# Optimization experiments

Measured on AMD Instinct MI355X. Metric: run time of the kernel, lower is better.

## Reference

```python
import jax, jax.numpy as jnp
import numpy as np

MODES = 12

def _conv3x3_circular(x, w, b):
    # x: [B,C,H,W], w: [O,I,3,3] -> circular padding of 1 then VALID conv
    xp = jnp.pad(x, ((0, 0), (0, 0), (1, 1), (1, 1)), mode='wrap')
    y = jax.lax.conv_general_dilated(xp, w, window_strides=(1, 1), padding='VALID',
                                     dimension_numbers=('NCHW', 'OIHW', 'NCHW'))
    return y + b[None, :, None, None]

def _spectral_conv(x, w1, w2):
    # x: [B,C,H,W] real; w1, w2: [C,O,m1,m2] complex
    B, C, H, W = x.shape
    x_ft = jnp.fft.rfft2(x)  # [B,C,H,W//2+1] complex
    m1 = min(MODES, H // 2)
    m2 = min(MODES, W // 2 + 1)
    top = jnp.einsum('bixy,ioxy->boxy', x_ft[:, :, :m1, :m2], w1[:, :, :m1, :m2])
    bot = jnp.einsum('bixy,ioxy->boxy', x_ft[:, :, -m1:, :m2], w2[:, :, :m1, :m2])
    out_ft = jnp.zeros((B, w1.shape[1], H, W // 2 + 1), dtype=x_ft.dtype)
    out_ft = out_ft.at[:, :, :m1, :m2].set(top).at[:, :, -m1:, :m2].set(bot)
    return jnp.fft.irfft2(out_ft, s=(H, W))

def setup_inputs() -> dict:
    key = jax.random.key(0)
    ks = jax.random.split(key, 16)
    width = 32
    scale = 1.0 / (width * width)
    return {
        'x': jax.random.normal(ks[0], (64, 2, 128, 128), dtype=jnp.float32),
        'p_w': jax.random.normal(ks[1], (width, 2, 3, 3), dtype=jnp.float32) * 0.2,
        'p_b': jax.random.normal(ks[2], (width,), dtype=jnp.float32) * 0.1,
        'scw1r': jax.random.uniform(ks[3], (4, width, width, MODES, MODES), dtype=jnp.float32) * scale,
        'scw1i': jax.random.uniform(ks[4], (4, width, width, MODES, MODES), dtype=jnp.float32) * scale,
        'scw2r': jax.random.uniform(ks[5], (4, width, width, MODES, MODES), dtype=jnp.float32) * scale,
        'scw2i': jax.random.uniform(ks[6], (4, width, width, MODES, MODES), dtype=jnp.float32) * scale,
        'ww': jax.random.normal(ks[7], (4, width, width), dtype=jnp.float32) * (1.0 / np.sqrt(width)),
        'wb': jax.random.normal(ks[8], (4, width), dtype=jnp.float32) * 0.1,
        'q1_w': jax.random.normal(ks[9], (128, width), dtype=jnp.float32) * (1.0 / np.sqrt(width)),
        'q1_b': jax.random.normal(ks[10], (128,), dtype=jnp.float32) * 0.1,
        'q2_w': jax.random.normal(ks[11], (1, 128), dtype=jnp.float32) * (1.0 / np.sqrt(128.0)),
        'q2_b': jax.random.normal(ks[12], (1,), dtype=jnp.float32) * 0.1,
    }

def reference(x, p_w, p_b, scw1r, scw1i, scw2r, scw2i, ww, wb, q1_w, q1_b, q2_w, q2_b):
    h = _conv3x3_circular(x, p_w, p_b)  # lifting: [B,2,H,W] -> [B,width,H,W]
    for i in range(4):
        w1 = scw1r[i] + 1j * scw1i[i]
        w2 = scw2r[i] + 1j * scw2i[i]
        x1 = _spectral_conv(h, w1, w2)
        x2 = jnp.einsum('bihw,oi->bohw', h, ww[i]) + wb[i][None, :, None, None]
        h = jax.nn.gelu(x1 + x2, approximate=False)
    g = h.mean(axis=(2, 3))  # [B,width]
    g = jax.nn.gelu(g @ q1_w.T + q1_b, approximate=False)
    g = g @ q2_w.T + q2_b
    return jax.nn.sigmoid(g)
```

## Files before the change

### kernel.cpp

```cpp
#include <hip/hip_runtime.h>
#include <math.h>

#define B 64
#define CIN 2
#define CH 32
#define H 128
#define W 128
#define MODES 12
#define KY 24
#define KX 12
#define HW (H*W)
#define NMODE (KY*KX)

typedef float f32x2 __attribute__((ext_vector_type(2)));
__device__ __forceinline__ f32x2 mk2(float a, float b) { f32x2 r; r.x = a; r.y = b; return r; }

__device__ __forceinline__ float gelu_f(float x) {
    float ax = fabsf(x) * 0.70710678118654752f;
    float t  = __builtin_amdgcn_rcpf(1.0f + 0.3275911f * ax);
    float p  = t * (0.254829592f + t * (-0.284496736f + t * (1.421413741f +
               t * (-1.453152027f + t * 1.061405429f))));
    float e  = __expf(-ax * ax);
    float er = copysignf(1.0f - p * e, x);
    return 0.5f * x * (1.0f + er);
}

__global__ __launch_bounds__(256) void k_init_tables(
        float* cWkw, float* sWkw, float* cnsWkw,
        float* cnsH2, float* mnsH2) {
    int t = blockIdx.x * 256 + threadIdx.x;
    const float TWO_PI_OVER = 6.283185307179586476925f / 128.0f;
    if (t < MODES * W) {
        int k = t / W, w = t % W;
        int m = (k * w) & 127;
        float s, c;
        sincosf(TWO_PI_OVER * (float)m, &s, &c);
        cWkw[k * W + w] = c;  sWkw[k * W + w] = s;
        cnsWkw[(k * W + w) * 2]     = c;
        cnsWkw[(k * W + w) * 2 + 1] = -s;
    } else if (t < MODES * W + KY * H) {
        int u = t - MODES * W;
        int kyI = u / H, hh = u % H;
        int ky = (kyI < MODES) ? kyI : (H - MODES + (kyI - MODES));
        int m = (ky * hh) & 127;
        float s, c;
        sincosf(TWO_PI_OVER * (float)m, &s, &c);
        cnsH2[(hh * KY + kyI) * 2]     = c;
        cnsH2[(hh * KY + kyI) * 2 + 1] = s;
        mnsH2[(hh * KY + kyI) * 2]     = -s;
        mnsH2[(hh * KY + kyI) * 2 + 1] = c;
    }
}

__global__ __launch_bounds__(256) void k_reorder_w(
        const float* __restrict__ w1r, const float* __restrict__ w1i,
        const float* __restrict__ w2r, const float* __restrict__ w2i,
        float* __restrict__ wR) {
    int idx = blockIdx.x * 256 + threadIdx.x;
    if (idx >= 4 * NMODE * CH * CH) return;
    int o = idx & 31;
    int i = (idx >> 5) & 31;
    int m = (idx >> 10) % NMODE;
    int layer = idx / (NMODE * CH * CH);
    int kyI = m / KX, kx = m % KX;
    const float *sr, *si;
    int row;
    if (kyI < MODES) { sr = w1r; si = w1i; row = kyI; }
    else             { sr = w2r; si = w2i; row = kyI - MODES; }
    int src = ((layer * CH + i) * CH + o) * (MODES * MODES) + row * MODES + kx;
    wR[(size_t)idx * 2]     = sr[src];
    wR[(size_t)idx * 2 + 1] = si[src];
}

__global__ __launch_bounds__(256) void k_transpose_ww(
        const float* __restrict__ ww, float* __restrict__ wwT) {
    int idx = blockIdx.x * 256 + threadIdx.x;
    if (idx >= 4 * CH * CH) return;
    int l = idx / (CH * CH);
    int r = idx % (CH * CH);
    int i = r / CH, o = r % CH;
    wwT[idx] = ww[l * CH * CH + o * CH + i];
}

__global__ __launch_bounds__(128) void k_lift(
        const float* __restrict__ x, const float* __restrict__ pw,
        const float* __restrict__ pb, float* __restrict__ h) {
    int bh = blockIdx.x;
    int b = bh >> 7, hr = bh & 127;
    int w = threadIdx.x;
    int wl = (w + W - 1) & (W - 1), wr2 = (w + 1) & (W - 1);
    float xv[CIN][3][3];
    #pragma unroll
    for (int ic = 0; ic < CIN; ++ic) {
        const float* xc = x + (size_t)(b * CIN + ic) * HW;
        #pragma unroll
        for (int r = 0; r < 3; ++r) {
            int hh = (hr + r - 1 + H) & (H - 1);
            const float* xr = xc + hh * W;
            xv[ic][r][0] = xr[wl];
            xv[ic][r][1] = xr[w];
            xv[ic][r][2] = xr[wr2];
        }
    }
    for (int o = 0; o < CH; ++o) {
        float acc = pb[o];
        const float* wo = pw + o * CIN * 9;
        #pragma unroll
        for (int ic = 0; ic < CIN; ++ic)
            #pragma unroll
            for (int r = 0; r < 3; ++r)
                #pragma unroll
                for (int c3 = 0; c3 < 3; ++c3)
                    acc += xv[ic][r][c3] * wo[ic * 9 + r * 3 + c3];
        h[(size_t)(b * CH + o) * HW + hr * W + w] = acc;
    }
}

__global__ __launch_bounds__(256) void k_dft_w(
        const float* __restrict__ h, const float* __restrict__ cnsWkw,
        float* __restrict__ Xw) {
    __shared__ float xs[64 * 129];
    int row0 = blockIdx.x * 64;
    int tid = threadIdx.x;
    const float4* src = (const float4*)(h + (size_t)row0 * W);
    #pragma unroll
    for (int it = 0; it < 8; ++it) {
        int idx = it * 256 + tid;
        int r = idx >> 5, c4 = idx & 31;
        float4 v = src[idx];
        float* d = xs + r * 129 + c4 * 4;
        d[0] = v.x; d[1] = v.y; d[2] = v.z; d[3] = v.w;
    }
    __syncthreads();
    int r = tid & 63;
    int kp = __builtin_amdgcn_readfirstlane(tid >> 6);
    const f32x2* tw = (const f32x2*)cnsWkw + kp * 3 * W;
    f32x2 a0 = mk2(0.f, 0.f), a1 = mk2(0.f, 0.f), a2 = mk2(0.f, 0.f);
    const float* xr = xs + r * 129;
    #pragma unroll 4
    for (int w = 0; w < W; ++w) {
        float xv = xr[w];
        f32x2 x2 = mk2(xv, xv);
        a0 += x2 * tw[w];
        a1 += x2 * tw[W + w];
        a2 += x2 * tw[2 * W + w];
    }
    float2* dst = (float2*)(Xw + (size_t)(row0 + r) * MODES * 2) + kp * 3;
    dst[0] = make_float2(a0.x, a0.y);
    dst[1] = make_float2(a1.x, a1.y);
    dst[2] = make_float2(a2.x, a2.y);
}

__global__ __launch_bounds__(320) void k_dft_h(
        const float* __restrict__ Xw, const float* __restrict__ cnsH2,
        float* __restrict__ Xf) {
    __shared__ float4 xs4[H * KX / 2];
    const float2* xs = (const float2*)xs4;
    int bc = blockIdx.x;
    int tid = threadIdx.x;
    const float4* src = (const float4*)(Xw + (size_t)bc * H * KX * 2);
    #pragma unroll
    for (int r = 0; r < 3; ++r) {
        int idx = r * 320 + tid;
        if (idx < H * KX / 2) xs4[idx] = src[idx];
    }
    __syncthreads();
    if (tid < KY * KX) {
        int ky = tid / KX, kx = tid % KX;
        const float2* cs = (const float2*)cnsH2 + ky;
        float ar = 0.f, ai = 0.f;
        #pragma unroll 4
        for (int hh = 0; hh < H; ++hh) {
            float2 v = xs[hh * KX + kx];
            float2 t = cs[hh * KY];
            ar += v.x * t.x + v.y * t.y;
            ai += v.y * t.x - v.x * t.y;
        }
        ((float2*)Xf)[(size_t)tid * (B * CH) + bc] = make_float2(ar, ai);
    }
}

__global__ __launch_bounds__(256) void k_specmul(
        const float* __restrict__ Xf, const float* __restrict__ wRl,
        float* __restrict__ Yt) {
    int m = blockIdx.x;
    int o = threadIdx.x & 31;
    int bq = threadIdx.x >> 5;
    const f32x2* X  = (const f32x2*)Xf  + (size_t)m * (B * CH);
    const f32x2* Wm = (const f32x2*)wRl + (size_t)m * (CH * CH);
    f32x2 acc2[8];
    #pragma unroll
    for (int j = 0; j < 8; ++j) acc2[j] = mk2(0.f, 0.f);
    for (int i = 0; i < CH; ++i) {
        f32x2 wv  = Wm[i * CH + o];
        f32x2 wvB = mk2(-wv.y, wv.x);
        #pragma unroll
        for (int j = 0; j < 8; ++j) {
            f32x2 xv = X[(bq * 8 + j) * CH + i];
            acc2[j] += mk2(xv.x, xv.x) * wv + mk2(xv.y, xv.y) * wvB;
        }
    }
    float2* Yp = (float2*)Yt;
    #pragma unroll
    for (int j = 0; j < 8; ++j)
        Yp[((size_t)(bq * 8 + j) * NMODE + m) * CH + o] = make_float2(acc2[j].x, acc2[j].y);
}

__global__ __launch_bounds__(384) void k_idft_h(
        const float* __restrict__ Yt, const float* __restrict__ cnsH2,
        const float* __restrict__ mnsH2, float* __restrict__ Zt) {
    int b = blockIdx.x;
    int hh0 = blockIdx.y * 16;
    int o = threadIdx.x & 31;
    int kx = threadIdx.x >> 5;
    float yr[KY], yi[KY];
    #pragma unroll
    for (int ky = 0; ky < KY; ++ky) {
        float2 v = ((const float2*)Yt)[((size_t)b * NMODE + ky * KX + kx) * CH + o];
        yr[ky] = v.x;  yi[ky] = v.y;
    }
    float sc = (kx == 0 ? 1.0f : 2.0f) / (float)HW;
    #pragma unroll 2
    for (int hr = 0; hr < 16; ++hr) {
        int hh = hh0 + hr;
        const f32x2* cs = (const f32x2*)(cnsH2 + hh * KY * 2);
        const f32x2* ms = (const f32x2*)(mnsH2 + hh * KY * 2);
        f32x2 a = mk2(0.f, 0.f);
        #pragma unroll
        for (int ky = 0; ky < KY; ++ky)
            a += mk2(yr[ky], yr[ky]) * cs[ky] + mk2(yi[ky], yi[ky]) * ms[ky];
        size_t base = ((size_t)(b * H + hh) * 2) * (KX * CH) + kx * CH + o;
        Zt[base]            = a.x * sc;
        Zt[base + KX * CH]  = a.y * sc;
    }
}

template <int LAST>
__global__ __launch_bounds__(512, 4) void k_fused(
        float* __restrict__ h, const float* __restrict__ Zt,
        const float* __restrict__ wwT, const float* __restrict__ wb,
        const float* __restrict__ cWkw, const float* __restrict__ sWkw,
        float* __restrict__ part) {
    __shared__ float hs[CH * W];
    __shared__ float red[8][8];
    int bh = blockIdx.x;
    int b = bh >> 7, hr = bh & 127;
    int tid = threadIdx.x;
    int w = tid & 127;
    int og = __builtin_amdgcn_readfirstlane(tid >> 7);
    const float* hrow = h + (size_t)b * CH * HW + hr * W;
    #pragma unroll
    for (int r = 0; r < 2; ++r) {
        int f4 = r * 512 + tid;
        int i = f4 >> 5;
        int col = (f4 & 31) * 4;
        float4 v = *(const float4*)(hrow + (size_t)i * HW + col);
        *(float4*)(hs + i * W + col) = v;
    }
    float ck[MODES], nsk[MODES];
    #pragma unroll
    for (int k = 0; k < MODES; ++k) {
        ck[k]  = cWkw[k * W + w];
        nsk[k] = -sWkw[k * W + w];
    }
    float acc[8];
    const float* wbo = wb + og * 8;
    #pragma unroll
    for (int j = 0; j < 8; ++j) acc[j] = wbo[j];
    __syncthreads();
    #pragma unroll 4
    for (int i = 0; i < CH; ++i) {
        float hv = hs[i * W + w];
        const float* wt = wwT + i * CH + og * 8;
        #pragma unroll
        for (int j = 0; j < 8; ++j) acc[j] += hv * wt[j];
    }
    const float* Zb = Zt + ((size_t)bh * 2) * (KX * CH) + og * 8;
    #pragma unroll
    for (int k = 0; k < MODES; ++k) {
        const float* zr = Zb + k * CH;
        const float* zi = zr + KX * CH;
        float ckv = ck[k], nskv = nsk[k];
        #pragma unroll
        for (int j = 0; j < 8; ++j)
            acc[j] += zr[j] * ckv + zi[j] * nskv;
    }
    if (LAST == 0) {
        float* hout = h + (size_t)(b * CH + og * 8) * HW + hr * W + w;
        #pragma unroll
        for (int j = 0; j < 8; ++j)
            hout[(size_t)j * HW] = gelu_f(acc[j]);
    } else {
        float v[8];
        #pragma unroll
        for (int j = 0; j < 8; ++j) v[j] = gelu_f(acc[j]);
        #pragma unroll
        for (int j = 0; j < 8; ++j)
            #pragma unroll
            for (int off = 32; off > 0; off >>= 1)
                v[j] += __shfl_xor(v[j], off, 64);
        int wave = tid >> 6;
        if ((tid & 63) == 0) {
            #pragma unroll
            for (int j = 0; j < 8; ++j) red[wave][j] = v[j];
        }
        __syncthreads();
        if (tid < CH) {
            float p = red[2 * (tid >> 3)][tid & 7] + red[2 * (tid >> 3) + 1][tid & 7];
            part[((size_t)b * CH + tid) * H + hr] = p;
        }
    }
}

__global__ __launch_bounds__(64) void k_reduce(
        const float* __restrict__ part, float* __restrict__ g) {
    int bc = blockIdx.x;
    int t = threadIdx.x;
    float s = part[(size_t)bc * H + t] + part[(size_t)bc * H + 64 + t];
    #pragma unroll
    for (int off = 32; off > 0; off >>= 1) s += __shfl_down(s, off, 64);
    if (t == 0) g[bc] = s * (1.0f / (float)HW);
}

__global__ __launch_bounds__(128) void k_head(
        const float* __restrict__ g, const float* __restrict__ q1w,
        const float* __restrict__ q1b, const float* __restrict__ q2w,
        const float* __restrict__ q2b, float* __restrict__ out) {
    __shared__ float gs[CH];
    __shared__ float red2[2];
    int b = blockIdx.x;
    int t = threadIdx.x;
    if (t < CH) gs[t] = g[b * CH + t];
    __syncthreads();
    float a = q1b[t];
    #pragma unroll
    for (int c = 0; c < CH; ++c) a += gs[c] * q1w[t * CH + c];
    a = gelu_f(a);
    float hsum = a * q2w[t];
    #pragma unroll
    for (int off = 32; off > 0; off >>= 1) hsum += __shfl_down(hsum, off, 64);
    if ((t & 63) == 0) red2[t >> 6] = hsum;
    __syncthreads();
    if (t == 0) {
        float logit = red2[0] + red2[1] + q2b[0];
        out[b] = 1.0f / (1.0f + expf(-logit));
    }
}

extern "C" void kernel_launch(void* const* d_in, const int* in_sizes, int n_in,
                              void* d_out, int out_size, void* d_ws, size_t ws_size,
                              hipStream_t stream) {
    const float* x   = (const float*)d_in[0];
    const float* p_w = (const float*)d_in[1];
    const float* p_b = (const float*)d_in[2];
    const float* w1r = (const float*)d_in[3];
    const float* w1i = (const float*)d_in[4];
    const float* w2r = (const float*)d_in[5];
    const float* w2i = (const float*)d_in[6];
    const float* ww  = (const float*)d_in[7];
    const float* wb  = (const float*)d_in[8];
    const float* q1w = (const float*)d_in[9];
    const float* q1b = (const float*)d_in[10];
    const float* q2w = (const float*)d_in[11];
    const float* q2b = (const float*)d_in[12];
    float* out = (float*)d_out;

    float* ws = (float*)d_ws;
    size_t off = 0;
    auto alloc = [&](size_t n) {
        float* p = ws + off;
        off += (n + 63) & ~(size_t)63;
        return p;
    };
    float* cWkw   = alloc(MODES * W);
    float* sWkw   = alloc(MODES * W);
    float* cnsWkw = alloc(MODES * W * 2);
    float* cnsH2  = alloc(H * KY * 2);
    float* mnsH2  = alloc(H * KY * 2);
    float* hBuf = alloc((size_t)B * CH * HW);
    float* XwZ  = alloc((size_t)B * CH * H * KX * 2);
    float* Xf   = alloc((size_t)NMODE * B * CH * 2);
    float* Yt   = alloc((size_t)B * NMODE * CH * 2);
    float* wR   = alloc((size_t)4 * NMODE * CH * CH * 2);
    float* wwT  = alloc(4 * CH * CH);
    float* part = alloc((size_t)B * CH * H);
    float* g    = alloc(B * CH);

    k_init_tables<<<(MODES * W + KY * H + 255) / 256, 256, 0, stream>>>(
        cWkw, sWkw, cnsWkw, cnsH2, mnsH2);
    k_reorder_w<<<(4 * NMODE * CH * CH + 255) / 256, 256, 0, stream>>>(
        w1r, w1i, w2r, w2i, wR);
    k_transpose_ww<<<(4 * CH * CH + 255) / 256, 256, 0, stream>>>(ww, wwT);

    k_lift<<<B * H, 128, 0, stream>>>(x, p_w, p_b, hBuf);

    for (int layer = 0; layer < 4; ++layer) {
        k_dft_w<<<(B * CH * H) / 64, 256, 0, stream>>>(hBuf, cnsWkw, XwZ);
        k_dft_h<<<B * CH, 320, 0, stream>>>(XwZ, cnsH2, Xf);
        k_specmul<<<NMODE, 256, 0, stream>>>(
            Xf, wR + (size_t)layer * NMODE * CH * CH * 2, Yt);
        k_idft_h<<<dim3(B, 8), 384, 0, stream>>>(Yt, cnsH2, mnsH2, XwZ);
        if (layer < 3)
            k_fused<0><<<B * H, 512, 0, stream>>>(
                hBuf, XwZ, wwT + layer * CH * CH, wb + layer * CH, cWkw, sWkw, part);
        else
            k_fused<1><<<B * H, 512, 0, stream>>>(
                hBuf, XwZ, wwT + layer * CH * CH, wb + layer * CH, cWkw, sWkw, part);
    }

    k_reduce<<<B * CH, 64, 0, stream>>>(part, g);
    k_head<<<B, 128, 0, stream>>>(g, q1w, q1b, q2w, q2b, out);
}
```

Measured before the change: 804.9 us.

## Give each k_dft_w thread six modes with w-major twiddles; pack k_fused math

k_dft_w now runs 128-thread blocks where each thread accumulates six frequency modes instead of three. The twiddle table is relaid out w-major so the six twiddles per column sit next to each other, and each shared-memory load of x is reused across more modes. k_fused now uses float2 packed vectors for the pointwise channel mix and inverse-W accumulation, aiming at packed FMA instructions. The change trades fewer waves per block and more registers per thread for less redundant loading.

```diff
diff --git a/kernel.cpp b/kernel.cpp
--- a/kernel.cpp
+++ b/kernel.cpp
@@ -26,7 +26,7 @@
 }
 
 __global__ __launch_bounds__(256) void k_init_tables(
-        float* cWkw, float* sWkw, float* cnsWkw,
+        float* cWkw, float* sWkw, float* cnsWwk,
         float* cnsH2, float* mnsH2) {
     int t = blockIdx.x * 256 + threadIdx.x;
     const float TWO_PI_OVER = 6.283185307179586476925f / 128.0f;
@@ -36,8 +36,8 @@
         float s, c;
         sincosf(TWO_PI_OVER * (float)m, &s, &c);
         cWkw[k * W + w] = c;  sWkw[k * W + w] = s;
-        cnsWkw[(k * W + w) * 2]     = c;
-        cnsWkw[(k * W + w) * 2 + 1] = -s;
+        cnsWwk[(w * MODES + k) * 2]     = c;
+        cnsWwk[(w * MODES + k) * 2 + 1] = -s;
     } else if (t < MODES * W + KY * H) {
         int u = t - MODES * W;
         int kyI = u / H, hh = u % H;
@@ -116,16 +116,16 @@
     }
 }
 
-__global__ __launch_bounds__(256) void k_dft_w(
-        const float* __restrict__ h, const float* __restrict__ cnsWkw,
+__global__ __launch_bounds__(128) void k_dft_w(
+        const float* __restrict__ h, const float* __restrict__ cnsWwk,
         float* __restrict__ Xw) {
     __shared__ float xs[64 * 129];
     int row0 = blockIdx.x * 64;
     int tid = threadIdx.x;
     const float4* src = (const float4*)(h + (size_t)row0 * W);
     #pragma unroll
-    for (int it = 0; it < 8; ++it) {
-        int idx = it * 256 + tid;
+    for (int it = 0; it < 16; ++it) {
+        int idx = it * 128 + tid;
         int r = idx >> 5, c4 = idx & 31;
         float4 v = src[idx];
         float* d = xs + r * 129 + c4 * 4;
@@ -134,21 +134,21 @@
     __syncthreads();
     int r = tid & 63;
     int kp = __builtin_amdgcn_readfirstlane(tid >> 6);
-    const f32x2* tw = (const f32x2*)cnsWkw + kp * 3 * W;
-    f32x2 a0 = mk2(0.f, 0.f), a1 = mk2(0.f, 0.f), a2 = mk2(0.f, 0.f);
+    const f32x2* tw = (const f32x2*)cnsWwk + kp * 6;
+    f32x2 a0 = mk2(0.f, 0.f), a1 = a0, a2 = a0, a3 = a0, a4 = a0, a5 = a0;
     const float* xr = xs + r * 129;
     #pragma unroll 4
     for (int w = 0; w < W; ++w) {
         float xv = xr[w];
         f32x2 x2 = mk2(xv, xv);
-        a0 += x2 * tw[w];
-        a1 += x2 * tw[W + w];
-        a2 += x2 * tw[2 * W + w];
-    }
-    float2* dst = (float2*)(Xw + (size_t)(row0 + r) * MODES * 2) + kp * 3;
-    dst[0] = make_float2(a0.x, a0.y);
-    dst[1] = make_float2(a1.x, a1.y);
-    dst[2] = make_float2(a2.x, a2.y);
+        const f32x2* t = tw + w * MODES;
+        a0 += x2 * t[0];  a1 += x2 * t[1];  a2 += x2 * t[2];
+        a3 += x2 * t[3];  a4 += x2 * t[4];  a5 += x2 * t[5];
+    }
+    float2* dst = (float2*)(Xw + (size_t)(row0 + r) * MODES * 2) + kp * 6;
+    dst[0] = make_float2(a0.x, a0.y);  dst[1] = make_float2(a1.x, a1.y);
+    dst[2] = make_float2(a2.x, a2.y);  dst[3] = make_float2(a3.x, a3.y);
+    dst[4] = make_float2(a4.x, a4.y);  dst[5] = make_float2(a5.x, a5.y);
 }
 
 __global__ __launch_bounds__(320) void k_dft_h(
@@ -263,37 +263,44 @@
         ck[k]  = cWkw[k * W + w];
         nsk[k] = -sWkw[k * W + w];
     }
-    float acc[8];
-    const float* wbo = wb + og * 8;
-    #pragma unroll
-    for (int j = 0; j < 8; ++j) acc[j] = wbo[j];
+    f32x2 acc2[4];
+    const f32x2* wb2 = (const f32x2*)(wb + og * 8);
+    #pragma unroll
+    for (int j = 0; j < 4; ++j) acc2[j] = wb2[j];
     __syncthreads();
     #pragma unroll 4
     for (int i = 0; i < CH; ++i) {
         float hv = hs[i * W + w];
-        const float* wt = wwT + i * CH + og * 8;
-        #pragma unroll
-        for (int j = 0; j < 8; ++j) acc[j] += hv * wt[j];
+        f32x2 hv2 = mk2(hv, hv);
+        const f32x2* wt2 = (const f32x2*)(wwT + i * CH + og * 8);
+        #pragma unroll
+        for (int j = 0; j < 4; ++j) acc2[j] += hv2 * wt2[j];
     }
     const float* Zb = Zt + ((size_t)bh * 2) * (KX * CH) + og * 8;
     #pragma unroll
     for (int k = 0; k < MODES; ++k) {
-        const float* zr = Zb + k * CH;
-        const float* zi = zr + KX * CH;
-        float ckv = ck[k], nskv = nsk[k];
-        #pragma unroll
-        for (int j = 0; j < 8; ++j)
-            acc[j] += zr[j] * ckv + zi[j] * nskv;
+        const f32x2* zr2 = (const f32x2*)(Zb + k * CH);
+        const f32x2* zi2 = (const f32x2*)(Zb + k * CH + KX * CH);
+        f32x2 ck2  = mk2(ck[k], ck[k]);
+        f32x2 nsk2 = mk2(nsk[k], nsk[k]);
+        #pragma unroll
+        for (int j = 0; j < 4; ++j)
+            acc2[j] += zr2[j] * ck2 + zi2[j] * nsk2;
     }
     if (LAST == 0) {
         float* hout = h + (size_t)(b * CH + og * 8) * HW + hr * W + w;
         #pragma unroll
-        for (int j = 0; j < 8; ++j)
-            hout[(size_t)j * HW] = gelu_f(acc[j]);
+        for (int j = 0; j < 4; ++j) {
+            hout[(size_t)(2 * j)     * HW] = gelu_f(acc2[j].x);
+            hout[(size_t)(2 * j + 1) * HW] = gelu_f(acc2[j].y);
+        }
     } else {
         float v[8];
         #pragma unroll
-        for (int j = 0; j < 8; ++j) v[j] = gelu_f(acc[j]);
+        for (int j = 0; j < 4; ++j) {
+            v[2 * j]     = gelu_f(acc2[j].x);
+            v[2 * j + 1] = gelu_f(acc2[j].y);
+        }
         #pragma unroll
         for (int j = 0; j < 8; ++j)
             #pragma unroll
@@ -374,7 +381,7 @@
     };
     float* cWkw   = alloc(MODES * W);
     float* sWkw   = alloc(MODES * W);
-    float* cnsWkw = alloc(MODES * W * 2);
+    float* cnsWwk = alloc(W * MODES * 2);
     float* cnsH2  = alloc(H * KY * 2);
     float* mnsH2  = alloc(H * KY * 2);
     float* hBuf = alloc((size_t)B * CH * HW);
@@ -387,7 +394,7 @@
     float* g    = alloc(B * CH);
 
     k_init_tables<<<(MODES * W + KY * H + 255) / 256, 256, 0, stream>>>(
-        cWkw, sWkw, cnsWkw, cnsH2, mnsH2);
+        cWkw, sWkw, cnsWwk, cnsH2, mnsH2);
     k_reorder_w<<<(4 * NMODE * CH * CH + 255) / 256, 256, 0, stream>>>(
         w1r, w1i, w2r, w2i, wR);
     k_transpose_ww<<<(4 * CH * CH + 255) / 256, 256, 0, stream>>>(ww, wwT);
@@ -395,7 +402,7 @@
     k_lift<<<B * H, 128, 0, stream>>>(x, p_w, p_b, hBuf);
 
     for (int layer = 0; layer < 4; ++layer) {
-        k_dft_w<<<(B * CH * H) / 64, 256, 0, stream>>>(hBuf, cnsWkw, XwZ);
+        k_dft_w<<<(B * CH * H) / 64, 128, 0, stream>>>(hBuf, cnsWwk, XwZ);
         k_dft_h<<<B * CH, 320, 0, stream>>>(XwZ, cnsH2, Xf);
         k_specmul<<<NMODE, 256, 0, stream>>>(
             Xf, wR + (size_t)layer * NMODE * CH * CH * 2, Yt);
```

Measured after the change: 836.9 us. 1.04x slower.
